# Kernel tuning notes

Hardware: AMD Instinct MI355X
Metric: run time of the kernel (lower is better)

The kernel has to match this reference:

```python
import jax, jax.numpy as jnp
import numpy as np

RADIUS = 10  # watermark_radius
EPS = 1e-5   # BatchNorm eps

def _conv(x, w, b, g, be, m, v):
    # Conv2d 3x3 pad 1 + BatchNorm(eval) + ReLU, NCHW
    y = jax.lax.conv_general_dilated(x, w, (1, 1), 'SAME',
                                     dimension_numbers=('NCHW', 'OIHW', 'NCHW'))
    y = y + b[None, :, None, None]
    y = g[None, :, None, None] * (y - m[None, :, None, None]) * jax.lax.rsqrt(v + EPS)[None, :, None, None] + be[None, :, None, None]
    return jax.nn.relu(y)

def _watermark_indices(C, H, W, L, r):
    # Replicates the (channel, i, j) iteration order of the torch loop.
    chs, ys, xs = [], [], []
    cy0, cx0 = H // 2, W // 2
    for c in range(C):
        for i in range(-r, r + 1):
            for j in range(-r, r + 1):
                if len(chs) >= L:
                    return np.array(chs), np.array(ys), np.array(xs)
                y, x = cy0 + i, cx0 + j
                if 0 <= y < H and 0 <= x < W and i * i + j * j <= r * r:
                    chs.append(c); ys.append(y); xs.append(x)
    return np.array(chs), np.array(ys), np.array(xs)

def setup_inputs() -> dict:
    key = jax.random.key(0)
    ks = jax.random.split(key, 8)
    B, Cc, H, W, L = 16, 64, 256, 256, 256
    s = 0.05  # weight scale for numerical stability
    inp = {
        'image': jax.random.normal(ks[0], (B, 3, H, W), jnp.float32),
        'message': jax.random.uniform(ks[1], (B, L), jnp.float32),
        'w0': jax.random.normal(ks[2], (Cc, 3, 3, 3), jnp.float32) * s,
        'b0': jnp.zeros((Cc,), jnp.float32),
        'g0': jnp.ones((Cc,), jnp.float32),
        'be0': jnp.zeros((Cc,), jnp.float32),
        'm0': jnp.zeros((Cc,), jnp.float32),
        'v0': jnp.ones((Cc,), jnp.float32),
        'wk': jax.random.normal(ks[3], (3, Cc, Cc, 3, 3), jnp.float32) * s,
        'bk': jnp.zeros((3, Cc), jnp.float32),
        'gk': jnp.ones((3, Cc), jnp.float32),
        'bek': jnp.zeros((3, Cc), jnp.float32),
        'mk': jnp.zeros((3, Cc), jnp.float32),
        'vk': jnp.ones((3, Cc), jnp.float32),
        'wa': jax.random.normal(ks[4], (Cc, Cc + 3 + L, 3, 3), jnp.float32) * s,
        'ba': jnp.zeros((Cc,), jnp.float32),
        'ga': jnp.ones((Cc,), jnp.float32),
        'bea': jnp.zeros((Cc,), jnp.float32),
        'ma': jnp.zeros((Cc,), jnp.float32),
        'va': jnp.ones((Cc,), jnp.float32),
        'wf': jax.random.normal(ks[5], (3, Cc, 1, 1), jnp.float32) * s,
        'bf': jnp.zeros((3,), jnp.float32),
    }
    return inp

def reference(image, message, w0, b0, g0, be0, m0, v0,
              wk, bk, gk, bek, mk, vk,
              wa, ba, ga, bea, ma, va, wf, bf):
    B, _, H, W = image.shape
    L = message.shape[1]
    # conv stack
    x = _conv(image, w0, b0, g0, be0, m0, v0)
    for t in range(wk.shape[0]):
        x = _conv(x, wk[t], bk[t], gk[t], bek[t], mk[t], vk[t])
    C = x.shape[1]
    # FFT2 over spatial dims
    fft = jnp.fft.fft2(x.astype(jnp.complex64))
    # vectorized tree-ring watermark scatter (precomputed static indices)
    ch, yy, xx = _watermark_indices(C, H, W, L, RADIUS)
    vals = message[:, :ch.shape[0]]                      # [B, L]
    cvals = (vals + 1j * vals).astype(jnp.complex64)     # complex(value, value)
    fft = fft.at[:, ch, yy, xx].set(cvals)
    enc = jnp.fft.ifft2(fft).real.astype(image.dtype)
    # concat [expanded message, encoded, image]
    msg = jnp.broadcast_to(message[:, :, None, None], (B, L, H, W))
    cat = jnp.concatenate([msg, enc, image], axis=1)
    y = _conv(cat, wa, ba, ga, bea, ma, va)
    # final 1x1 conv
    out = jnp.einsum('bchw,oc->bohw', y, wf[:, :, 0, 0]) + bf[None, :, None, None]
    return out
```

## Files before the change

### kernel.cpp

```cpp
#include <hip/hip_runtime.h>
#include <hip/hip_bf16.h>

#define HH 256
#define WW 256
#define NB 16
#define CC 64
#define NL 256
#define HWSZ (HH*WW)
#define EPSV 1e-5f
#define NYK 16
#define YK0 118

using bf16 = __hip_bfloat16;
using short8  = __attribute__((ext_vector_type(8))) short;
using floatx4 = __attribute__((ext_vector_type(4))) float;

__device__ __forceinline__ ushort f2b(float f){
    bf16 h = __float2bfloat16(f);
    union { bf16 h; ushort u; } cv; cv.h = h; return cv.u;
}
__device__ __forceinline__ float b2fu(ushort u){
    union { unsigned int i; float f; } cv; cv.i = ((unsigned int)u) << 16; return cv.f;
}

__global__ void prep_w_k(const float* __restrict__ wk, const float* __restrict__ wa,
                         ushort* __restrict__ wkb2, ushort* __restrict__ wab2)
{
    int i = blockIdx.x*256 + threadIdx.x;
    const int NWK = 3*9*64*64, NWA = 19*2048;
    if (i < NWK) {
        int ci8 = i & 7; int r = i >> 3;
        int lane = r & 63; r >>= 6;
        int mi = r & 3; r >>= 2;
        int g = r % 18; int t = r / 18;
        int q = g / 6, kc2 = (g / 3) & 1, p = g % 3;
        int quad = lane >> 4, n16 = lane & 15;
        int co = mi*16 + n16, ci = kc2*32 + quad*8 + ci8, tap = p*3 + q;
        wkb2[i] = f2b(wk[(((size_t)t*64 + co)*64 + ci)*9 + tap]);
    } else if (i < NWK + NWA) {
        int i2 = i - NWK;
        int ci8 = i2 & 7; int r = i2 >> 3;
        int lane = r & 63; r >>= 6;
        int mi = r & 3; int g = r >> 2;
        int quad = lane >> 4, n16 = lane & 15;
        int co = mi*16 + n16;
        float v = 0.f;
        if (g < 18) {
            int q = g/6, kc2 = (g/3)&1, p = g%3;
            int ci = kc2*32 + quad*8 + ci8, tap = p*3 + q;
            v = wa[((size_t)co*323 + 256 + ci)*9 + tap];
        } else {
            int j = quad*8 + ci8;
            if (j < 27) {
                int ci = j/9, rem = j%9;
                v = wa[((size_t)co*323 + 320 + ci)*9 + rem];
            }
        }
        wab2[i2] = f2b(v);
    }
}

#define LDAF(DST, G) { const ushort* bp = wbase + (size_t)(G)*2048;            \
    _Pragma("unroll") for (int mi_=0; mi_<4; mi_++)                            \
        DST[mi_] = *(const short8*)(bp + mi_*512); }

#define MFMA_GRP(AF, BF, P)                                                    \
    _Pragma("unroll") for (int mi_=0; mi_<4; mi_++) {                          \
      _Pragma("unroll") for (int ni_=0; ni_<4; ni_++)                          \
        acc[mi_][ni_] = __builtin_amdgcn_mfma_f32_16x16x32_bf16(               \
            AF[mi_], BF[ni_+(P)], acc[mi_][ni_], 0, 0, 0); }

__global__ __launch_bounds__(256) void conv0_k(
    const float* __restrict__ img, const float* __restrict__ w0,
    const float* __restrict__ bias, const float* __restrict__ gamma,
    const float* __restrict__ beta, const float* __restrict__ mean,
    const float* __restrict__ var, ushort* __restrict__ outp)
{
    __shared__ float s_i[3][18][18];
    __shared__ float s_wv[64*27];
    __shared__ float s_al[64], s_be[64];
    __shared__ ushort __align__(16) s_y[256*72];

    int tid = threadIdx.x;
    int x0 = blockIdx.x*16, y0 = blockIdx.y*16, b = blockIdx.z;
    if (tid < 64) {
        float a = gamma[tid]*rsqrtf(var[tid]+EPSV);
        s_al[tid] = a; s_be[tid] = (bias[tid]-mean[tid])*a + beta[tid];
    }
    for (int c = tid; c < 64*27; c += 256) s_wv[c] = w0[c];
    for (int c = tid; c < 3*18*18; c += 256) {
        int ci = c / 324, pp = c % 324, py = pp/18, px = pp%18;
        int gy = y0-1+py, gx = x0-1+px;
        float v = 0.f;
        if ((unsigned)gy < 256u && (unsigned)gx < 256u)
            v = img[((size_t)b*3 + ci)*HWSZ + gy*256 + gx];
        s_i[ci][py][px] = v;
    }
    __syncthreads();

    int ly = tid >> 4, lx = tid & 15;
    float xv[27];
    #pragma unroll
    for (int ci=0;ci<3;ci++)
      #pragma unroll
      for (int p=0;p<3;p++)
        #pragma unroll
        for (int q=0;q<3;q++)
            xv[ci*9+p*3+q] = s_i[ci][ly+p][lx+q];

    for (int co=0; co<64; co++) {
        float a = 0.f;
        #pragma unroll
        for (int j=0;j<27;j++) a += xv[j]*s_wv[co*27+j];
        s_y[tid*72 + co] = f2b(fmaxf(s_al[co]*a + s_be[co], 0.f));
    }
    __syncthreads();
    size_t obase = (size_t)b*HWSZ*64;
    for (int c = tid; c < 256*8; c += 256) {
        int ci8 = c & 7, px = c >> 3;
        int gy = y0 + (px>>4), gx = x0 + (px&15);
        *(uint4*)&outp[obase + (size_t)(gy*256+gx)*64 + ci8*8] =
            *(const uint4*)&s_y[px*72 + ci8*8];
    }
}

__global__ __launch_bounds__(256,3) void convm_k(
    const ushort* __restrict__ in, const ushort* __restrict__ wgt,
    ushort* __restrict__ outp,
    const float* __restrict__ gamma, const float* __restrict__ beta,
    const float* __restrict__ mean,  const float* __restrict__ var,
    const float* __restrict__ bias,  float* __restrict__ plane)
{
    __shared__ ushort __align__(16) s_x[18*18*72];
    __shared__ float s_al[64], s_be[64];

    const int tid = threadIdx.x;
    const int x0 = blockIdx.x*16, y0 = blockIdx.y*16, b = blockIdx.z;

    if (tid < 64) {
        float a = gamma[tid]*rsqrtf(var[tid]+EPSV);
        s_al[tid] = a; s_be[tid] = (bias[tid]-mean[tid])*a + beta[tid];
    }
    const size_t ibase = (size_t)b*HWSZ*64;
    for (int c = tid; c < 18*18*8; c += 256) {
        int ci8 = c & 7, pp = c >> 3;
        int px = pp % 18, py = pp / 18;
        int gy = y0-1+py, gx = x0-1+px;
        uint4 v = make_uint4(0,0,0,0);
        if ((unsigned)gy < 256u && (unsigned)gx < 256u)
            v = *(const uint4*)&in[ibase + (size_t)(gy*256+gx)*64 + ci8*8];
        *(uint4*)&s_x[(py*18+px)*72 + ci8*8] = v;
    }
    __syncthreads();

    const int lane = tid & 63, wid = tid >> 6;
    const int n16 = lane & 15, quad = lane >> 4;
    const ushort* wbase = wgt + (size_t)lane*8;

    floatx4 acc[4][4];
    #pragma unroll
    for (int mi=0;mi<4;mi++)
      #pragma unroll
      for (int ni=0;ni<4;ni++)
        #pragma unroll
        for (int r=0;r<4;r++) acc[mi][ni][r] = 0.f;

    short8 afA[4], afB[4], bfA[6], bfB[6];

    LDAF(afA, 0);
    #pragma unroll
    for (int rr=0; rr<6; rr++)
        bfA[rr] = *(const short8*)&s_x[((wid*4+rr)*18 + n16)*72 + quad*8];

    #pragma unroll
    for (int g=0; g<18; g++) {
        const int p = g % 3, j = g / 3;
        if (g+1 < 18) {
            if (g & 1) { LDAF(afA, g+1); } else { LDAF(afB, g+1); }
        }
        if (p == 0 && j+1 < 6) {
            const int nq = (j+1) >> 1, nk = (j+1) & 1;
            if (j & 1) {
                #pragma unroll
                for (int rr=0; rr<6; rr++)
                    bfA[rr] = *(const short8*)&s_x[((wid*4+rr)*18 + n16 + nq)*72 + nk*32 + quad*8];
            } else {
                #pragma unroll
                for (int rr=0; rr<6; rr++)
                    bfB[rr] = *(const short8*)&s_x[((wid*4+rr)*18 + n16 + nq)*72 + nk*32 + quad*8];
            }
        }
        if (g & 1) { if (j & 1) { MFMA_GRP(afB, bfB, p) } else { MFMA_GRP(afB, bfA, p) } }
        else       { if (j & 1) { MFMA_GRP(afA, bfB, p) } else { MFMA_GRP(afA, bfA, p) } }
    }
    __syncthreads();

    ushort* s_y = s_x;
    #pragma unroll
    for (int mi=0;mi<4;mi++)
      #pragma unroll
      for (int ni=0;ni<4;ni++) {
        int px = (wid*4+ni)*16 + n16;
        int cob = mi*16 + quad*4;
        ushort u[4];
        #pragma unroll
        for (int r=0;r<4;r++) {
            float y = fmaxf(s_al[cob+r]*acc[mi][ni][r] + s_be[cob+r], 0.f);
            u[r] = f2b(y);
            if (plane && mi==0 && quad==0 && r==0)
                plane[(size_t)b*HWSZ + (y0+wid*4+ni)*256 + x0 + n16] = y;
        }
        uint2 pk; pk.x = (uint)u[0] | ((uint)u[1]<<16); pk.y = (uint)u[2] | ((uint)u[3]<<16);
        *(uint2*)&s_y[px*72 + cob] = pk;
      }
    __syncthreads();
    for (int c = tid; c < 256*8; c += 256) {
        int ci8 = c & 7, px = c >> 3;
        int gy = y0 + (px>>4), gx = x0 + (px&15);
        *(uint4*)&outp[ibase + (size_t)(gy*256+gx)*64 + ci8*8] =
            *(const uint4*)&s_y[px*72 + ci8*8];
    }
}

__global__ __launch_bounds__(256,2) void conva_k(
    const ushort* __restrict__ enc, const float* __restrict__ img,
    const float* __restrict__ dplane, const ushort* __restrict__ wgt,
    const float* __restrict__ gamma, const float* __restrict__ beta,
    const float* __restrict__ mean,  const float* __restrict__ var,
    const float* __restrict__ bias,
    const float* __restrict__ Tb,
    const float* __restrict__ wf, const float* __restrict__ bfv,
    float* __restrict__ outp)
{
    __shared__ ushort __align__(16) s_x[18*18*72];
    __shared__ float s_al[64], s_be[64];
    __shared__ float s_T[64*9];
    __shared__ float s_wf[3*64];
    __shared__ float s_bf[3];

    const int tid = threadIdx.x;
    const int x0 = blockIdx.x*16, y0 = blockIdx.y*16, b = blockIdx.z;

    if (tid < 64) {
        float a = gamma[tid]*rsqrtf(var[tid]+EPSV);
        s_al[tid] = a; s_be[tid] = (bias[tid]-mean[tid])*a + beta[tid];
    }
    if (tid < 192) s_wf[tid] = wf[tid];
    if (tid < 3)   s_bf[tid] = bfv[tid];
    for (int c = tid; c < 64*9; c += 256) s_T[c] = Tb[(size_t)b*576 + c];

    const int lane = tid & 63, wid = tid >> 6;
    const int n16 = lane & 15, quad = lane >> 4;
    const ushort* wbase = wgt + (size_t)lane*8;

    const size_t ibase = (size_t)b*HWSZ*64;
    for (int c = tid; c < 18*18*8; c += 256) {
        int ci8 = c & 7, pp = c >> 3;
        int px = pp % 18, py = pp / 18;
        int gy = y0-1+py, gx = x0-1+px;
        uint4 v = make_uint4(0,0,0,0);
        if ((unsigned)gy < 256u && (unsigned)gx < 256u) {
            v = *(const uint4*)&enc[ibase + (size_t)(gy*256+gx)*64 + ci8*8];
            if (ci8 == 0) {
                float d = dplane[(size_t)b*HWSZ + gy*256 + gx];
                ushort nb = f2b(b2fu((ushort)(v.x & 0xffffu)) + d);
                v.x = (v.x & 0xffff0000u) | (uint)nb;
            }
        }
        *(uint4*)&s_x[(py*18+px)*72 + ci8*8] = v;
    }

    short8 bimg[4];
    #pragma unroll
    for (int ni=0; ni<4; ni++) {
        short8 t;
        #pragma unroll
        for (int ci8=0; ci8<8; ci8++) {
            int j = quad*8 + ci8;
            float v = 0.f;
            if (j < 27) {
                int ci = j/9, rem = j%9, p = rem/3, q = rem%3;
                int gy = y0 + wid*4 + ni + p - 1, gx = x0 + n16 + q - 1;
                if ((unsigned)gy < 256u && (unsigned)gx < 256u)
                    v = img[((size_t)b*3 + ci)*HWSZ + gy*256 + gx];
            }
            t[ci8] = (short)f2b(v);
        }
        bimg[ni] = t;
    }
    __syncthreads();

    floatx4 acc[4][4];
    #pragma unroll
    for (int mi=0;mi<4;mi++)
      #pragma unroll
      for (int ni=0;ni<4;ni++)
        #pragma unroll
        for (int r=0;r<4;r++) acc[mi][ni][r] = 0.f;

    short8 afA[4], afB[4], bf[6];

    LDAF(afA, 0);
    #pragma unroll
    for (int g=0; g<18; g++) {
        const int p = g % 3, j = g / 3;
        if (g & 1) { LDAF(afA, g+1); } else { LDAF(afB, g+1); }
        if (p == 0) {
            const int nq = j >> 1, nk = j & 1;
            #pragma unroll
            for (int rr=0; rr<6; rr++)
                bf[rr] = *(const short8*)&s_x[((wid*4+rr)*18 + n16 + nq)*72 + nk*32 + quad*8];
        }
        if (g & 1) { MFMA_GRP(afB, bf, p) } else { MFMA_GRP(afA, bf, p) }
    }
    #pragma unroll
    for (int mi=0;mi<4;mi++)
      #pragma unroll
      for (int ni=0;ni<4;ni++)
        acc[mi][ni] = __builtin_amdgcn_mfma_f32_16x16x32_bf16(
            afA[mi], bimg[ni], acc[mi][ni], 0, 0, 0);

    float po[3][4];
    #pragma unroll
    for (int o=0;o<3;o++)
      #pragma unroll
      for (int ni=0;ni<4;ni++) po[o][ni] = 0.f;

    #pragma unroll
    for (int mi=0;mi<4;mi++) {
        int cob = mi*16 + quad*4;
        #pragma unroll
        for (int r=0;r<4;r++) {
            int co = cob + r;
            float al = s_al[co], be = s_be[co];
            const float* t = &s_T[co*9];
            float w0f = s_wf[0*64+co], w1f = s_wf[1*64+co], w2f = s_wf[2*64+co];
            #pragma unroll
            for (int ni=0;ni<4;ni++) {
                int h = y0 + wid*4 + ni, w = x0 + n16;
                float tv = t[0];
                if (h==0)   tv -= t[1];
                if (h==255) tv -= t[2];
                if (w==0)   tv -= t[3];
                if (w==255) tv -= t[4];
                if (h==0   && w==0)   tv += t[5];
                if (h==0   && w==255) tv += t[6];
                if (h==255 && w==0)   tv += t[7];
                if (h==255 && w==255) tv += t[8];
                float y = fmaxf(al*(acc[mi][ni][r] + tv) + be, 0.f);
                po[0][ni] += w0f*y; po[1][ni] += w1f*y; po[2][ni] += w2f*y;
            }
        }
    }
    #pragma unroll
    for (int o=0;o<3;o++)
      #pragma unroll
      for (int ni=0;ni<4;ni++) {
        float pv = po[o][ni];
        pv += __shfl_xor(pv, 16, 64);
        pv += __shfl_xor(pv, 32, 64);
        if (quad == o) {
            int h = y0 + wid*4 + ni, w = x0 + n16;
            outp[((size_t)b*3 + o)*HWSZ + h*256 + w] = pv + s_bf[o];
        }
      }
}

__global__ __launch_bounds__(256) void msgterm_k(const float* __restrict__ msg,
                                                 const float* __restrict__ wa,
                                                 float* __restrict__ Tbuf)
{
    __shared__ float red[256];
    int b = blockIdx.x, o = blockIdx.y, l = threadIdx.x;
    float m = msg[b*NL + l];
    float wv[9];
    #pragma unroll
    for (int t=0;t<9;t++) wv[t] = wa[((size_t)o*323 + l)*9 + t] * m;
    float comp[9];
    comp[0] = wv[0]+wv[1]+wv[2]+wv[3]+wv[4]+wv[5]+wv[6]+wv[7]+wv[8];
    comp[1] = wv[0]+wv[1]+wv[2];
    comp[2] = wv[6]+wv[7]+wv[8];
    comp[3] = wv[0]+wv[3]+wv[6];
    comp[4] = wv[2]+wv[5]+wv[8];
    comp[5] = wv[0]; comp[6]=wv[2]; comp[7]=wv[6]; comp[8]=wv[8];
    for (int cpi=0;cpi<9;cpi++){
        red[l] = comp[cpi];
        __syncthreads();
        for (int s=128;s>0;s>>=1){ if (l<s) red[l]+=red[l+s]; __syncthreads(); }
        if (l==0) Tbuf[((size_t)b*CC+o)*9+cpi] = red[0];
        __syncthreads();
    }
}

__global__ void build_idx_k(int* __restrict__ idx)
{
    if (threadIdx.x==0 && blockIdx.x==0) {
        int n=0;
        for (int i=-10;i<=10;i++)
            for (int j=-10;j<=10;j++) {
                if (n>=NL) return;
                if (i*i+j*j<=100) { idx[2*n]=128+i; idx[2*n+1]=128+j; n++; }
            }
    }
}

__global__ __launch_bounds__(256) void colA_k(const float* __restrict__ plane,
                                              float* __restrict__ Cbuf)
{
    __shared__ float twc[256], tws[256];
    int t = blockIdx.x, b = blockIdx.y, w = threadIdx.x;
    float sv, cv;
    __sincosf(6.283185307179586f * (float)w / 256.0f, &sv, &cv);
    twc[w]=cv; tws[w]=sv;
    __syncthreads();
    int yk = YK0 + t;
    const float* pb = &plane[(size_t)b*HWSZ];
    int m = 0;
    float fr=0.f, fi=0.f;
    for (int h=0; h<256; h++) {
        float xv = pb[h*256 + w];
        fr += xv*twc[m];
        fi -= xv*tws[m];
        m = (m + yk) & 255;
    }
    float* Cb = &Cbuf[((size_t)(b*NYK + t)*2)*256];
    Cb[w]       = fr;
    Cb[256 + w] = fi;
}

__global__ __launch_bounds__(256) void freqB_k(const float* __restrict__ Cbuf,
                                               const float* __restrict__ msg,
                                               const int* __restrict__ idx,
                                               float* __restrict__ D)
{
    __shared__ float twc[256], tws[256];
    __shared__ float sfr[4], sfi[4];
    int k = blockIdx.x, b = blockIdx.y, w = threadIdx.x;
    float sv, cv;
    __sincosf(6.283185307179586f * (float)w / 256.0f, &sv, &cv);
    twc[w]=cv; tws[w]=sv;
    __syncthreads();
    int yk = idx[2*k], xk = idx[2*k+1];
    int t = yk - YK0;
    const float* Cb = &Cbuf[((size_t)(b*NYK + t)*2)*256];
    float Cr = Cb[w], Ci = Cb[256 + w];
    int ang = (xk*w) & 255;
    float cx = twc[ang], sx = tws[ang];
    float fr = Cr*cx + Ci*sx;
    float fi = Ci*cx - Cr*sx;
    #pragma unroll
    for (int off=32; off>0; off>>=1) {
        fr += __shfl_xor(fr, off, 64);
        fi += __shfl_xor(fi, off, 64);
    }
    if ((w & 63) == 0) { sfr[w>>6] = fr; sfi[w>>6] = fi; }
    __syncthreads();
    if (w == 0) {
        float FR = sfr[0]+sfr[1]+sfr[2]+sfr[3];
        float FI = sfi[0]+sfi[1]+sfi[2]+sfi[3];
        float mv = msg[b*NL + k];
        D[((size_t)b*NL + k)*2 + 0] = mv - FR;
        D[((size_t)b*NL + k)*2 + 1] = mv - FI;
    }
}

__global__ __launch_bounds__(256) void rowC_k(const int* __restrict__ idx,
                                              const float* __restrict__ D,
                                              float* __restrict__ Sbuf)
{
    __shared__ float twc[256], tws[256], dr[256], di[256];
    __shared__ int iy[256], ix[256];
    int t = blockIdx.x, b = blockIdx.y, w = threadIdx.x;
    float sv, cv;
    __sincosf(6.283185307179586f * (float)w / 256.0f, &sv, &cv);
    twc[w]=cv; tws[w]=sv;
    dr[w] = D[((size_t)b*NL + w)*2+0];
    di[w] = D[((size_t)b*NL + w)*2+1];
    iy[w] = idx[2*w]; ix[w] = idx[2*w+1];
    __syncthreads();
    int yk = YK0 + t;
    float Sr=0.f, Si=0.f;
    for (int k=0;k<256;k++) {
        if (iy[k] != yk) continue;
        int ang = (ix[k]*w) & 255;
        float c = twc[ang], s = tws[ang];
        Sr += dr[k]*c - di[k]*s;
        Si += dr[k]*s + di[k]*c;
    }
    float* Sb = &Sbuf[((size_t)(b*NYK + t)*2)*256];
    Sb[w]       = Sr;
    Sb[256 + w] = Si;
}

__global__ __launch_bounds__(256) void applyD_k(const float* __restrict__ Sbuf,
                                                float* __restrict__ dplane)
{
    __shared__ float twc[256], tws[256];
    int h = blockIdx.x, b = blockIdx.y, w = threadIdx.x;
    float sv, cv;
    __sincosf(6.283185307179586f * (float)w / 256.0f, &sv, &cv);
    twc[w]=cv; tws[w]=sv;
    __syncthreads();
    float acc = 0.f;
    #pragma unroll
    for (int t=0;t<NYK;t++) {
        int yk = YK0 + t;
        int ang = (yk*h) & 255;
        float cy = twc[ang], sy = tws[ang];
        const float* Sb = &Sbuf[((size_t)(b*NYK + t)*2)*256];
        acc += cy*Sb[w] - sy*Sb[256 + w];
    }
    dplane[(size_t)b*HWSZ + h*256 + w] = acc * (1.0f/65536.0f);
}

extern "C" void kernel_launch(void* const* d_in, const int* in_sizes, int n_in,
                              void* d_out, int out_size, void* d_ws, size_t ws_size,
                              hipStream_t stream)
{
    const float* image = (const float*)d_in[0];
    const float* msg   = (const float*)d_in[1];
    const float* w0    = (const float*)d_in[2];
    const float* b0    = (const float*)d_in[3];
    const float* g0    = (const float*)d_in[4];
    const float* be0   = (const float*)d_in[5];
    const float* m0    = (const float*)d_in[6];
    const float* v0    = (const float*)d_in[7];
    const float* wk    = (const float*)d_in[8];
    const float* bk    = (const float*)d_in[9];
    const float* gk    = (const float*)d_in[10];
    const float* bek   = (const float*)d_in[11];
    const float* mk    = (const float*)d_in[12];
    const float* vk    = (const float*)d_in[13];
    const float* wa    = (const float*)d_in[14];
    const float* ba    = (const float*)d_in[15];
    const float* ga    = (const float*)d_in[16];
    const float* bea   = (const float*)d_in[17];
    const float* ma    = (const float*)d_in[18];
    const float* va    = (const float*)d_in[19];
    const float* wf    = (const float*)d_in[20];
    const float* bfv   = (const float*)d_in[21];
    float* out = (float*)d_out;

    char* base = (char*)d_ws;
    int*    idx    = (int*)base;
    float*  Dbuf   = (float*)(base + (4<<10));
    float*  Tbuf   = (float*)(base + (40<<10));
    ushort* wkb2   = (ushort*)(base + (128<<10));
    ushort* wab2   = (ushort*)(base + (384<<10));
    float*  Cbuf   = (float*)(base + (512<<10));
    float*  Sbuf   = (float*)(base + ((size_t)1<<20));
    float*  plane  = (float*)(base + ((size_t)2<<20));
    float*  dplane = (float*)(base + ((size_t)7<<20));
    ushort* bufA   = (ushort*)(base + ((size_t)12<<20));

    const size_t perB = (size_t)HWSZ*64*2*2;
    int chunk = 1;
    for (int c = NB; c >= 1; c >>= 1)
        if (((size_t)12<<20) + (size_t)c*perB <= ws_size) { chunk = c; break; }
    ushort* bufB = bufA + (size_t)chunk*HWSZ*64;

    build_idx_k<<<1,64,0,stream>>>(idx);
    msgterm_k<<<dim3(NB,CC),256,0,stream>>>(msg, wa, Tbuf);
    int prep_n = (3*9*64*64 + 19*2048 + 255)/256;
    prep_w_k<<<prep_n,256,0,stream>>>(wk, wa, wkb2, wab2);

    const size_t WL = (size_t)9*64*64;

    for (int cs = 0; cs < NB; cs += chunk) {
        dim3 g(16,16,chunk);
        const float* img_c = image + (size_t)cs*3*HWSZ;

        conv0_k<<<g,256,0,stream>>>(img_c, w0, b0, g0, be0, m0, v0, bufA);
        convm_k<<<g,256,0,stream>>>(bufA, wkb2 + 0*WL, bufB,
            gk+0*CC, bek+0*CC, mk+0*CC, vk+0*CC, bk+0*CC, nullptr);
        convm_k<<<g,256,0,stream>>>(bufB, wkb2 + 1*WL, bufA,
            gk+1*CC, bek+1*CC, mk+1*CC, vk+1*CC, bk+1*CC, nullptr);
        convm_k<<<g,256,0,stream>>>(bufA, wkb2 + 2*WL, bufB,
            gk+2*CC, bek+2*CC, mk+2*CC, vk+2*CC, bk+2*CC, plane);

        colA_k<<<dim3(NYK,chunk),256,0,stream>>>(plane, Cbuf);
        freqB_k<<<dim3(NL,chunk),256,0,stream>>>(Cbuf, msg + (size_t)cs*NL, idx, Dbuf);
        rowC_k<<<dim3(NYK,chunk),256,0,stream>>>(idx, Dbuf, Sbuf);
        applyD_k<<<dim3(HH,chunk),256,0,stream>>>(Sbuf, dplane);

        conva_k<<<g,256,0,stream>>>(bufB, img_c, dplane, wab2,
            ga, bea, ma, va, ba, Tbuf + (size_t)cs*CC*9, wf, bfv,
            out + (size_t)cs*3*HWSZ);
    }
}
```

Measured before the change: 888.0 us.

## Split input tile staging into channel halves and overlap upper half with MFMA

The 64-channel input tile for the 3x3 conv is now staged in two halves. The first 32 channels go to shared memory before compute starts. The upper 32 channels are loaded into registers and written to LDS during the first group of MFMAs, and the K-loop is reordered (GMAP) so all low-channel taps run first, with a barrier at group 6. This hides part of the global-load latency behind the first-half MFMA work, at the cost of more registers (six uint4 staging values) under a launch bound of three blocks, which could cause spills.

```diff
diff --git a/kernel.cpp b/kernel.cpp
--- a/kernel.cpp
+++ b/kernel.cpp
@@ -70,6 +70,8 @@
         acc[mi_][ni_] = __builtin_amdgcn_mfma_f32_16x16x32_bf16(               \
             AF[mi_], BF[ni_+(P)], acc[mi_][ni_], 0, 0, 0); }
 
+#define GMAP(G) ((((G)%9)/3)*6 + ((G)/9)*3 + ((G)%3))
+
 __global__ __launch_bounds__(256) void conv0_k(
     const float* __restrict__ img, const float* __restrict__ w0,
     const float* __restrict__ bias, const float* __restrict__ gamma,
@@ -142,16 +144,37 @@
         s_al[tid] = a; s_be[tid] = (bias[tid]-mean[tid])*a + beta[tid];
     }
     const size_t ibase = (size_t)b*HWSZ*64;
-    for (int c = tid; c < 18*18*8; c += 256) {
-        int ci8 = c & 7, pp = c >> 3;
-        int px = pp % 18, py = pp / 18;
-        int gy = y0-1+py, gx = x0-1+px;
+
+    #pragma unroll
+    for (int it = 0; it < 6; ++it) {
+        int c = tid + it*256;
+        if (c < 18*18*4) {
+            int ci4 = c & 3, pp = c >> 2;
+            int px = pp % 18, py = pp / 18;
+            int gy = y0-1+py, gx = x0-1+px;
+            uint4 v = make_uint4(0,0,0,0);
+            if ((unsigned)gy < 256u && (unsigned)gx < 256u)
+                v = *(const uint4*)&in[ibase + (size_t)(gy*256+gx)*64 + ci4*8];
+            *(uint4*)&s_x[(py*18+px)*72 + ci4*8] = v;
+        }
+    }
+    uint4 stgHi[6];
+    #pragma unroll
+    for (int it = 0; it < 6; ++it) {
+        int c = tid + it*256;
         uint4 v = make_uint4(0,0,0,0);
-        if ((unsigned)gy < 256u && (unsigned)gx < 256u)
-            v = *(const uint4*)&in[ibase + (size_t)(gy*256+gx)*64 + ci8*8];
-        *(uint4*)&s_x[(py*18+px)*72 + ci8*8] = v;
-    }
-    __syncthreads();
+        if (c < 18*18*4) {
+            int ci4 = c & 3, pp = c >> 2;
+            int px = pp % 18, py = pp / 18;
+            int gy = y0-1+py, gx = x0-1+px;
+            if ((unsigned)gy < 256u && (unsigned)gx < 256u)
+                v = *(const uint4*)&in[ibase + (size_t)(gy*256+gx)*64 + 32 + ci4*8];
+        }
+        stgHi[it] = v;
+    }
+    asm volatile("s_waitcnt lgkmcnt(0)" ::: "memory");
+    __builtin_amdgcn_s_barrier();
+    __builtin_amdgcn_sched_barrier(0);
 
     const int lane = tid & 63, wid = tid >> 6;
     const int n16 = lane & 15, quad = lane >> 4;
@@ -167,31 +190,47 @@
 
     short8 afA[4], afB[4], bfA[6], bfB[6];
 
-    LDAF(afA, 0);
+    LDAF(afA, GMAP(0));
     #pragma unroll
     for (int rr=0; rr<6; rr++)
         bfA[rr] = *(const short8*)&s_x[((wid*4+rr)*18 + n16)*72 + quad*8];
 
     #pragma unroll
-    for (int g=0; g<18; g++) {
-        const int p = g % 3, j = g / 3;
-        if (g+1 < 18) {
-            if (g & 1) { LDAF(afA, g+1); } else { LDAF(afB, g+1); }
-        }
-        if (p == 0 && j+1 < 6) {
-            const int nq = (j+1) >> 1, nk = (j+1) & 1;
-            if (j & 1) {
+    for (int gg=0; gg<18; ++gg) {
+        const int p = gg % 3, jp = gg / 3;
+        if (gg == 6) {
+            asm volatile("s_waitcnt lgkmcnt(0)" ::: "memory");
+            __builtin_amdgcn_s_barrier();
+            __builtin_amdgcn_sched_barrier(0);
+        }
+        if (gg + 1 < 18) {
+            if (gg & 1) { LDAF(afA, GMAP(gg+1)); } else { LDAF(afB, GMAP(gg+1)); }
+        }
+        if (p == 0 && jp + 1 < 6) {
+            const int kn = (jp+1) / 3, qn = (jp+1) % 3;
+            if (jp & 1) {
                 #pragma unroll
                 for (int rr=0; rr<6; rr++)
-                    bfA[rr] = *(const short8*)&s_x[((wid*4+rr)*18 + n16 + nq)*72 + nk*32 + quad*8];
+                    bfA[rr] = *(const short8*)&s_x[((wid*4+rr)*18 + n16 + qn)*72 + kn*32 + quad*8];
             } else {
                 #pragma unroll
                 for (int rr=0; rr<6; rr++)
-                    bfB[rr] = *(const short8*)&s_x[((wid*4+rr)*18 + n16 + nq)*72 + nk*32 + quad*8];
+                    bfB[rr] = *(const short8*)&s_x[((wid*4+rr)*18 + n16 + qn)*72 + kn*32 + quad*8];
             }
         }
-        if (g & 1) { if (j & 1) { MFMA_GRP(afB, bfB, p) } else { MFMA_GRP(afB, bfA, p) } }
-        else       { if (j & 1) { MFMA_GRP(afA, bfB, p) } else { MFMA_GRP(afA, bfA, p) } }
+        if (gg == 0) {
+            #pragma unroll
+            for (int it = 0; it < 6; ++it) {
+                int c = tid + it*256;
+                if (c < 18*18*4) {
+                    int ci4 = c & 3, pp = c >> 2;
+                    int px = pp % 18, py = pp / 18;
+                    *(uint4*)&s_x[(py*18+px)*72 + 32 + ci4*8] = stgHi[it];
+                }
+            }
+        }
+        if (gg & 1) { if (jp & 1) { MFMA_GRP(afB, bfB, p) } else { MFMA_GRP(afB, bfA, p) } }
+        else        { if (jp & 1) { MFMA_GRP(afA, bfB, p) } else { MFMA_GRP(afA, bfA, p) } }
     }
     __syncthreads();
 
```

After: 867.6 us. -2.3%, faster.

## Split convm input staging into two channel halves to halve LDS and raise occupancy

Applied to the files above, without the earlier changes.

The 3x3 conv kernel now stages its 18x18 input halo in LDS 32 channels at a time instead of all 64. This halves the shared-memory footprint, and launch bounds go from 3 to 4 blocks per CU. The output epilogue is also written in two channel halves through the smaller buffer. In exchange, the double-buffered A/B fragment prefetch is dropped and extra block-wide barriers are added, which exposes load latency between the MFMA groups.

```diff
diff --git a/kernel.cpp b/kernel.cpp
--- a/kernel.cpp
+++ b/kernel.cpp
@@ -124,14 +124,14 @@
     }
 }
 
-__global__ __launch_bounds__(256,3) void convm_k(
+__global__ __launch_bounds__(256,4) void convm_k(
     const ushort* __restrict__ in, const ushort* __restrict__ wgt,
     ushort* __restrict__ outp,
     const float* __restrict__ gamma, const float* __restrict__ beta,
     const float* __restrict__ mean,  const float* __restrict__ var,
     const float* __restrict__ bias,  float* __restrict__ plane)
 {
-    __shared__ ushort __align__(16) s_x[18*18*72];
+    __shared__ ushort __align__(16) s_x[18*18*36];
     __shared__ float s_al[64], s_be[64];
 
     const int tid = threadIdx.x;
@@ -142,16 +142,6 @@
         s_al[tid] = a; s_be[tid] = (bias[tid]-mean[tid])*a + beta[tid];
     }
     const size_t ibase = (size_t)b*HWSZ*64;
-    for (int c = tid; c < 18*18*8; c += 256) {
-        int ci8 = c & 7, pp = c >> 3;
-        int px = pp % 18, py = pp / 18;
-        int gy = y0-1+py, gx = x0-1+px;
-        uint4 v = make_uint4(0,0,0,0);
-        if ((unsigned)gy < 256u && (unsigned)gx < 256u)
-            v = *(const uint4*)&in[ibase + (size_t)(gy*256+gx)*64 + ci8*8];
-        *(uint4*)&s_x[(py*18+px)*72 + ci8*8] = v;
-    }
-    __syncthreads();
 
     const int lane = tid & 63, wid = tid >> 6;
     const int n16 = lane & 15, quad = lane >> 4;
@@ -165,60 +155,71 @@
         #pragma unroll
         for (int r=0;r<4;r++) acc[mi][ni][r] = 0.f;
 
-    short8 afA[4], afB[4], bfA[6], bfB[6];
-
-    LDAF(afA, 0);
-    #pragma unroll
-    for (int rr=0; rr<6; rr++)
-        bfA[rr] = *(const short8*)&s_x[((wid*4+rr)*18 + n16)*72 + quad*8];
-
-    #pragma unroll
-    for (int g=0; g<18; g++) {
-        const int p = g % 3, j = g / 3;
-        if (g+1 < 18) {
-            if (g & 1) { LDAF(afA, g+1); } else { LDAF(afB, g+1); }
-        }
-        if (p == 0 && j+1 < 6) {
-            const int nq = (j+1) >> 1, nk = (j+1) & 1;
-            if (j & 1) {
+    short8 af[4], bf[6];
+
+    #pragma unroll
+    for (int half=0; half<2; ++half) {
+        if (half == 1) __syncthreads();
+        #pragma unroll
+        for (int it = 0; it < 6; ++it) {
+            int c = tid + it*256;
+            if (c < 18*18*4) {
+                int ci4 = c & 3, pp = c >> 2;
+                int px = pp % 18, py = pp / 18;
+                int gy = y0-1+py, gx = x0-1+px;
+                uint4 v = make_uint4(0,0,0,0);
+                if ((unsigned)gy < 256u && (unsigned)gx < 256u)
+                    v = *(const uint4*)&in[ibase + (size_t)(gy*256+gx)*64 + half*32 + ci4*8];
+                *(uint4*)&s_x[pp*36 + ci4*8] = v;
+            }
+        }
+        __syncthreads();
+
+        #pragma unroll
+        for (int g3=0; g3<9; ++g3) {
+            const int q = g3/3, p = g3%3;
+            const int gsto = q*6 + half*3 + p;
+            if (p == 0) {
                 #pragma unroll
                 for (int rr=0; rr<6; rr++)
-                    bfA[rr] = *(const short8*)&s_x[((wid*4+rr)*18 + n16 + nq)*72 + nk*32 + quad*8];
-            } else {
-                #pragma unroll
-                for (int rr=0; rr<6; rr++)
-                    bfB[rr] = *(const short8*)&s_x[((wid*4+rr)*18 + n16 + nq)*72 + nk*32 + quad*8];
-            }
-        }
-        if (g & 1) { if (j & 1) { MFMA_GRP(afB, bfB, p) } else { MFMA_GRP(afB, bfA, p) } }
-        else       { if (j & 1) { MFMA_GRP(afA, bfB, p) } else { MFMA_GRP(afA, bfA, p) } }
+                    bf[rr] = *(const short8*)&s_x[((wid*4+rr)*18 + n16 + q)*36 + quad*8];
+            }
+            LDAF(af, gsto);
+            MFMA_GRP(af, bf, p);
+        }
     }
     __syncthreads();
 
     ushort* s_y = s_x;
     #pragma unroll
-    for (int mi=0;mi<4;mi++)
-      #pragma unroll
-      for (int ni=0;ni<4;ni++) {
-        int px = (wid*4+ni)*16 + n16;
-        int cob = mi*16 + quad*4;
-        ushort u[4];
-        #pragma unroll
-        for (int r=0;r<4;r++) {
-            float y = fmaxf(s_al[cob+r]*acc[mi][ni][r] + s_be[cob+r], 0.f);
-            u[r] = f2b(y);
-            if (plane && mi==0 && quad==0 && r==0)
-                plane[(size_t)b*HWSZ + (y0+wid*4+ni)*256 + x0 + n16] = y;
-        }
-        uint2 pk; pk.x = (uint)u[0] | ((uint)u[1]<<16); pk.y = (uint)u[2] | ((uint)u[3]<<16);
-        *(uint2*)&s_y[px*72 + cob] = pk;
-      }
-    __syncthreads();
-    for (int c = tid; c < 256*8; c += 256) {
-        int ci8 = c & 7, px = c >> 3;
-        int gy = y0 + (px>>4), gx = x0 + (px&15);
-        *(uint4*)&outp[ibase + (size_t)(gy*256+gx)*64 + ci8*8] =
-            *(const uint4*)&s_y[px*72 + ci8*8];
+    for (int h=0; h<2; ++h) {
+        #pragma unroll
+        for (int mi=2*h; mi<2*h+2; ++mi)
+          #pragma unroll
+          for (int ni=0; ni<4; ++ni) {
+            int px = (wid*4+ni)*16 + n16;
+            int cob = mi*16 + quad*4;
+            ushort u[4];
+            #pragma unroll
+            for (int r=0;r<4;r++) {
+                float y = fmaxf(s_al[cob+r]*acc[mi][ni][r] + s_be[cob+r], 0.f);
+                u[r] = f2b(y);
+                if (plane && mi==0 && quad==0 && r==0)
+                    plane[(size_t)b*HWSZ + (y0+wid*4+ni)*256 + x0 + n16] = y;
+            }
+            uint2 pk; pk.x = (uint)u[0] | ((uint)u[1]<<16); pk.y = (uint)u[2] | ((uint)u[3]<<16);
+            *(uint2*)&s_y[px*36 + (mi&1)*16 + quad*4] = pk;
+          }
+        __syncthreads();
+        #pragma unroll
+        for (int it=0; it<4; ++it) {
+            int c = tid + it*256;
+            int ci4 = c & 3, px = c >> 2;
+            int gy = y0 + (px>>4), gx = x0 + (px&15);
+            *(uint4*)&outp[ibase + (size_t)(gy*256+gx)*64 + h*32 + ci4*8] =
+                *(const uint4*)&s_y[px*36 + ci4*8];
+        }
+        if (h == 0) __syncthreads();
     }
 }
 
```

After: 1.047 ms. +17.9%, slower.

## Split output channels across two wave groups in convm and conva kernels

Applied to the files above, without the earlier changes.

Doubles the block size of the MFMA conv kernels to 512 threads. The two groups of four waves each compute half of the 64 output channels for the same 16x16 tile, which halves per-thread accumulators and A-fragment registers. The aim is higher occupancy and more waves to hide latency. In exchange, each wave still loads the full B fragments from shared memory, so LDS reads per output roughly double. The fused 1x1 output in conva now needs an extra shared-memory reduction across the two groups, with additional barriers.

```diff
diff --git a/kernel.cpp b/kernel.cpp
--- a/kernel.cpp
+++ b/kernel.cpp
@@ -60,12 +60,12 @@
     }
 }
 
-#define LDAF(DST, G) { const ushort* bp = wbase + (size_t)(G)*2048;            \
-    _Pragma("unroll") for (int mi_=0; mi_<4; mi_++)                            \
-        DST[mi_] = *(const short8*)(bp + mi_*512); }
-
-#define MFMA_GRP(AF, BF, P)                                                    \
-    _Pragma("unroll") for (int mi_=0; mi_<4; mi_++) {                          \
+#define LDAF2(DST, G) { const ushort* bp = wbase + (size_t)(G)*2048;           \
+    DST[0] = *(const short8*)(bp);                                             \
+    DST[1] = *(const short8*)(bp + 512); }
+
+#define MFMA_GRP2(AF, BF, P)                                                   \
+    _Pragma("unroll") for (int mi_=0; mi_<2; mi_++) {                          \
       _Pragma("unroll") for (int ni_=0; ni_<4; ni_++)                          \
         acc[mi_][ni_] = __builtin_amdgcn_mfma_f32_16x16x32_bf16(               \
             AF[mi_], BF[ni_+(P)], acc[mi_][ni_], 0, 0, 0); }
@@ -124,7 +124,7 @@
     }
 }
 
-__global__ __launch_bounds__(256,3) void convm_k(
+__global__ __launch_bounds__(512,4) void convm_k(
     const ushort* __restrict__ in, const ushort* __restrict__ wgt,
     ushort* __restrict__ outp,
     const float* __restrict__ gamma, const float* __restrict__ beta,
@@ -142,7 +142,7 @@
         s_al[tid] = a; s_be[tid] = (bias[tid]-mean[tid])*a + beta[tid];
     }
     const size_t ibase = (size_t)b*HWSZ*64;
-    for (int c = tid; c < 18*18*8; c += 256) {
+    for (int c = tid; c < 18*18*8; c += 512) {
         int ci8 = c & 7, pp = c >> 3;
         int px = pp % 18, py = pp / 18;
         int gy = y0-1+py, gx = x0-1+px;
@@ -153,21 +153,22 @@
     }
     __syncthreads();
 
-    const int lane = tid & 63, wid = tid >> 6;
+    const int lane = tid & 63, wv = tid >> 6;
+    const int wid = wv & 3, grp = wv >> 2;
     const int n16 = lane & 15, quad = lane >> 4;
-    const ushort* wbase = wgt + (size_t)lane*8;
-
-    floatx4 acc[4][4];
-    #pragma unroll
-    for (int mi=0;mi<4;mi++)
+    const ushort* wbase = wgt + (size_t)lane*8 + (size_t)grp*1024;
+
+    floatx4 acc[2][4];
+    #pragma unroll
+    for (int mi=0;mi<2;mi++)
       #pragma unroll
       for (int ni=0;ni<4;ni++)
         #pragma unroll
         for (int r=0;r<4;r++) acc[mi][ni][r] = 0.f;
 
-    short8 afA[4], afB[4], bfA[6], bfB[6];
-
-    LDAF(afA, 0);
+    short8 afA[2], afB[2], bfA[6], bfB[6];
+
+    LDAF2(afA, 0);
     #pragma unroll
     for (int rr=0; rr<6; rr++)
         bfA[rr] = *(const short8*)&s_x[((wid*4+rr)*18 + n16)*72 + quad*8];
@@ -176,7 +177,7 @@
     for (int g=0; g<18; g++) {
         const int p = g % 3, j = g / 3;
         if (g+1 < 18) {
-            if (g & 1) { LDAF(afA, g+1); } else { LDAF(afB, g+1); }
+            if (g & 1) { LDAF2(afA, g+1); } else { LDAF2(afB, g+1); }
         }
         if (p == 0 && j+1 < 6) {
             const int nq = (j+1) >> 1, nk = (j+1) & 1;
@@ -190,31 +191,32 @@
                     bfB[rr] = *(const short8*)&s_x[((wid*4+rr)*18 + n16 + nq)*72 + nk*32 + quad*8];
             }
         }
-        if (g & 1) { if (j & 1) { MFMA_GRP(afB, bfB, p) } else { MFMA_GRP(afB, bfA, p) } }
-        else       { if (j & 1) { MFMA_GRP(afA, bfB, p) } else { MFMA_GRP(afA, bfA, p) } }
+        if (g & 1) { if (j & 1) { MFMA_GRP2(afB, bfB, p) } else { MFMA_GRP2(afB, bfA, p) } }
+        else       { if (j & 1) { MFMA_GRP2(afA, bfB, p) } else { MFMA_GRP2(afA, bfA, p) } }
     }
     __syncthreads();
 
     ushort* s_y = s_x;
     #pragma unroll
-    for (int mi=0;mi<4;mi++)
+    for (int mi=0;mi<2;mi++)
       #pragma unroll
       for (int ni=0;ni<4;ni++) {
+        int ami = grp*2 + mi;
         int px = (wid*4+ni)*16 + n16;
-        int cob = mi*16 + quad*4;
+        int cob = ami*16 + quad*4;
         ushort u[4];
         #pragma unroll
         for (int r=0;r<4;r++) {
             float y = fmaxf(s_al[cob+r]*acc[mi][ni][r] + s_be[cob+r], 0.f);
             u[r] = f2b(y);
-            if (plane && mi==0 && quad==0 && r==0)
+            if (plane && ami==0 && quad==0 && r==0)
                 plane[(size_t)b*HWSZ + (y0+wid*4+ni)*256 + x0 + n16] = y;
         }
         uint2 pk; pk.x = (uint)u[0] | ((uint)u[1]<<16); pk.y = (uint)u[2] | ((uint)u[3]<<16);
         *(uint2*)&s_y[px*72 + cob] = pk;
       }
     __syncthreads();
-    for (int c = tid; c < 256*8; c += 256) {
+    for (int c = tid; c < 256*8; c += 512) {
         int ci8 = c & 7, px = c >> 3;
         int gy = y0 + (px>>4), gx = x0 + (px&15);
         *(uint4*)&outp[ibase + (size_t)(gy*256+gx)*64 + ci8*8] =
@@ -222,7 +224,7 @@
     }
 }
 
-__global__ __launch_bounds__(256,2) void conva_k(
+__global__ __launch_bounds__(512,4) void conva_k(
     const ushort* __restrict__ enc, const float* __restrict__ img,
     const float* __restrict__ dplane, const ushort* __restrict__ wgt,
     const float* __restrict__ gamma, const float* __restrict__ beta,
@@ -247,14 +249,15 @@
     }
     if (tid < 192) s_wf[tid] = wf[tid];
     if (tid < 3)   s_bf[tid] = bfv[tid];
-    for (int c = tid; c < 64*9; c += 256) s_T[c] = Tb[(size_t)b*576 + c];
-
-    const int lane = tid & 63, wid = tid >> 6;
+    for (int c = tid; c < 64*9; c += 512) s_T[c] = Tb[(size_t)b*576 + c];
+
+    const int lane = tid & 63, wv = tid >> 6;
+    const int wid = wv & 3, grp = wv >> 2;
     const int n16 = lane & 15, quad = lane >> 4;
-    const ushort* wbase = wgt + (size_t)lane*8;
+    const ushort* wbase = wgt + (size_t)lane*8 + (size_t)grp*1024;
 
     const size_t ibase = (size_t)b*HWSZ*64;
-    for (int c = tid; c < 18*18*8; c += 256) {
+    for (int c = tid; c < 18*18*8; c += 512) {
         int ci8 = c & 7, pp = c >> 3;
         int px = pp % 18, py = pp / 18;
         int gy = y0-1+py, gx = x0-1+px;
@@ -290,31 +293,31 @@
     }
     __syncthreads();
 
-    floatx4 acc[4][4];
-    #pragma unroll
-    for (int mi=0;mi<4;mi++)
+    floatx4 acc[2][4];
+    #pragma unroll
+    for (int mi=0;mi<2;mi++)
       #pragma unroll
       for (int ni=0;ni<4;ni++)
         #pragma unroll
         for (int r=0;r<4;r++) acc[mi][ni][r] = 0.f;
 
-    short8 afA[4], afB[4], bf[6];
-
-    LDAF(afA, 0);
+    short8 afA[2], afB[2], bf[6];
+
+    LDAF2(afA, 0);
     #pragma unroll
     for (int g=0; g<18; g++) {
         const int p = g % 3, j = g / 3;
-        if (g & 1) { LDAF(afA, g+1); } else { LDAF(afB, g+1); }
+        if (g & 1) { LDAF2(afA, g+1); } else { LDAF2(afB, g+1); }
         if (p == 0) {
             const int nq = j >> 1, nk = j & 1;
             #pragma unroll
             for (int rr=0; rr<6; rr++)
                 bf[rr] = *(const short8*)&s_x[((wid*4+rr)*18 + n16 + nq)*72 + nk*32 + quad*8];
         }
-        if (g & 1) { MFMA_GRP(afB, bf, p) } else { MFMA_GRP(afA, bf, p) }
-    }
-    #pragma unroll
-    for (int mi=0;mi<4;mi++)
+        if (g & 1) { MFMA_GRP2(afB, bf, p) } else { MFMA_GRP2(afA, bf, p) }
+    }
+    #pragma unroll
+    for (int mi=0;mi<2;mi++)
       #pragma unroll
       for (int ni=0;ni<4;ni++)
         acc[mi][ni] = __builtin_amdgcn_mfma_f32_16x16x32_bf16(
@@ -327,8 +330,8 @@
       for (int ni=0;ni<4;ni++) po[o][ni] = 0.f;
 
     #pragma unroll
-    for (int mi=0;mi<4;mi++) {
-        int cob = mi*16 + quad*4;
+    for (int mi=0;mi<2;mi++) {
+        int cob = (grp*2 + mi)*16 + quad*4;
         #pragma unroll
         for (int r=0;r<4;r++) {
             int co = cob + r;
@@ -356,14 +359,27 @@
     for (int o=0;o<3;o++)
       #pragma unroll
       for (int ni=0;ni<4;ni++) {
-        float pv = po[o][ni];
-        pv += __shfl_xor(pv, 16, 64);
-        pv += __shfl_xor(pv, 32, 64);
-        if (quad == o) {
+        po[o][ni] += __shfl_xor(po[o][ni], 16, 64);
+        po[o][ni] += __shfl_xor(po[o][ni], 32, 64);
+      }
+    __syncthreads();
+    float* s_red = (float*)s_x;
+    #pragma unroll
+    for (int o=0;o<3;o++)
+      #pragma unroll
+      for (int ni=0;ni<4;ni++)
+        if (grp == 1 && quad == o)
+            s_red[((wid*3+o)*4+ni)*16 + n16] = po[o][ni];
+    __syncthreads();
+    #pragma unroll
+    for (int o=0;o<3;o++)
+      #pragma unroll
+      for (int ni=0;ni<4;ni++)
+        if (grp == 0 && quad == o) {
             int h = y0 + wid*4 + ni, w = x0 + n16;
-            outp[((size_t)b*3 + o)*HWSZ + h*256 + w] = pv + s_bf[o];
-        }
-      }
+            outp[((size_t)b*3 + o)*HWSZ + h*256 + w] =
+                po[o][ni] + s_red[((wid*3+o)*4+ni)*16 + n16] + s_bf[o];
+        }
 }
 
 __global__ __launch_bounds__(256) void msgterm_k(const float* __restrict__ msg,
@@ -571,11 +587,11 @@
         const float* img_c = image + (size_t)cs*3*HWSZ;
 
         conv0_k<<<g,256,0,stream>>>(img_c, w0, b0, g0, be0, m0, v0, bufA);
-        convm_k<<<g,256,0,stream>>>(bufA, wkb2 + 0*WL, bufB,
+        convm_k<<<g,512,0,stream>>>(bufA, wkb2 + 0*WL, bufB,
             gk+0*CC, bek+0*CC, mk+0*CC, vk+0*CC, bk+0*CC, nullptr);
-        convm_k<<<g,256,0,stream>>>(bufB, wkb2 + 1*WL, bufA,
+        convm_k<<<g,512,0,stream>>>(bufB, wkb2 + 1*WL, bufA,
             gk+1*CC, bek+1*CC, mk+1*CC, vk+1*CC, bk+1*CC, nullptr);
-        convm_k<<<g,256,0,stream>>>(bufA, wkb2 + 2*WL, bufB,
+        convm_k<<<g,512,0,stream>>>(bufA, wkb2 + 2*WL, bufB,
             gk+2*CC, bek+2*CC, mk+2*CC, vk+2*CC, bk+2*CC, plane);
 
         colA_k<<<dim3(NYK,chunk),256,0,stream>>>(plane, Cbuf);
@@ -583,7 +599,7 @@
         rowC_k<<<dim3(NYK,chunk),256,0,stream>>>(idx, Dbuf, Sbuf);
         applyD_k<<<dim3(HH,chunk),256,0,stream>>>(Sbuf, dplane);
 
-        conva_k<<<g,256,0,stream>>>(bufB, img_c, dplane, wab2,
+        conva_k<<<g,512,0,stream>>>(bufB, img_c, dplane, wab2,
             ga, bea, ma, va, ba, Tbuf + (size_t)cs*CC*9, wf, bfv,
             out + (size_t)cs*3*HWSZ);
     }
```

Measured after the change: 802.0 us. -9.7%, faster.
